# Kernel optimization log

Measured on AMD Instinct MI355X. Metric: run time of the kernel, lower is better.

The kernel has to match this reference:

```python
import jax, jax.numpy as jnp
import numpy as np

ALPHA = 0.5
NUM_NB = 8


def setup_inputs() -> dict:
    key = jax.random.key(0)
    k1, k2 = jax.random.split(key)
    pc1 = jax.random.normal(k1, (4, 3, 8192), dtype=jnp.float32)
    pred_flow = jax.random.normal(k2, (4, 3, 8192), dtype=jnp.float32)
    return {"pc1": pc1, "pred_flow": pred_flow}


def reference(pc1, pred_flow):
    # pc1, pred_flow: [B, 3, N] -> [B, N, 3]
    B, _, N = pc1.shape
    k = NUM_NB
    p = jnp.transpose(pc1, (0, 2, 1))         # [B, N, 3]
    f = jnp.transpose(pred_flow, (0, 2, 1))   # [B, N, 3]

    sq = jnp.sum(p * p, axis=-1)
    sqrdist = sq[:, :, None] + sq[:, None, :] - 2.0 * jnp.einsum('bnd,bmd->bnm', p, p)

    # k+1 smallest (sorted ascending), drop self (first column)
    neg_d, kidx = jax.lax.top_k(-sqrdist, k + 1)  # descending in -d == ascending in d
    dists = -neg_d[:, :, 1:]                      # [B, N, k]
    kidx = kidx[:, :, 1:]                         # [B, N, k]
    dists = jnp.maximum(dists, 0.0)

    # softmax over all N*k weights per batch
    w = jax.nn.softmax(jnp.exp(-dists / ALPHA).reshape(B, N * k), axis=1)
    w = w.reshape(B, N, k)

    # gather neighbor flows: [B, N, k, 3]
    grouped = jnp.take_along_axis(f[:, None, :, :],
                                  kidx[:, :, :, None],
                                  axis=2)
    diff = jnp.linalg.norm(grouped - f[:, :, None, :], axis=3)  # [B, N, k]
    diff_flow = (N * w * diff).sum(axis=2)                      # [B, N]
    return jnp.mean(diff_flow)
```

## Files before the change

### kernel.cpp

```cpp
#include <hip/hip_runtime.h>
#include <hip/hip_bf16.h>
#include <math.h>

#define BATCH 4
#define NQ 8192
#define KNB 8
#define K1 9
#define TILE 1024
#define CAP 24
#define THSAMP 256
#define SPART 2
#define IDXMASK 8191u
#define KEYMASK 0xFFFFE000u
#define EPS_S 1e-3f

#define CHAIN9(KEY) { unsigned kk = (KEY); \
  _Pragma("unroll") \
  for (int j = 0; j < K1; ++j) { \
    unsigned lo = min(kk, nk[j]); unsigned hi = max(kk, nk[j]); \
    nk[j] = lo; kk = hi; } }

#define DRAIN(T0) { \
  for (int i = 0; i < cnt; ++i) { \
    int j = sbuf[base + i]; \
    float dx = qx - sx[j], dy = qy - sy[j], dz = qz - sz[j]; \
    float d = dx*dx + dy*dy + dz*dz; \
    unsigned key = (__float_as_uint(d) & KEYMASK) | (unsigned)(c0 + (T0) + j); \
    if (key < nk[K1-1]) CHAIN9(key); \
  } \
  cnt = 0; \
  if (nk[K1-1] != 0xFFFFFFFFu) { \
    float td = __uint_as_float(nk[K1-1] | 0x1FFFu); \
    thetaS = fminf(thetaS, 0.5f*(td - qq) + EPS_S); \
  } }

#define GPROC(SS, JLOCAL) { \
  if ((SS) <= thetaS) { sbuf[base + cnt] = (unsigned short)(JLOCAL); cnt++; } }

__global__ __launch_bounds__(256) void theta_kernel(
    const float* __restrict__ pc, unsigned* __restrict__ thetaOut,
    float* __restrict__ hOut)
{
  __shared__ float swx[THSAMP], swy[THSAMP], swz[THSAMP];
  const int b = blockIdx.y, p = blockIdx.z;
  const int q = blockIdx.x * 256 + threadIdx.x;
  const float* __restrict__ px = pc + (size_t)b * 3 * NQ;
  const float* __restrict__ py = px + NQ;
  const float* __restrict__ pz = px + 2 * NQ;
  const int tid = threadIdx.x;
  const int si = tid * (NQ / THSAMP) + p * (NQ / THSAMP / SPART);
  swx[tid] = px[si]; swy[tid] = py[si]; swz[tid] = pz[si];
  __syncthreads();
  const float qx = px[q], qy = py[q], qz = pz[q];
  if (p == 0) hOut[b * NQ + q] = 0.5f * (qx*qx + qy*qy + qz*qz);
  unsigned nk[K1];
#pragma unroll
  for (int j = 0; j < K1; ++j) nk[j] = 0xFFFFFFFFu;
  for (int i = 0; i < THSAMP; ++i) {
    float dx = qx - swx[i], dy = qy - swy[i], dz = qz - swz[i];
    float d = dx * dx + dy * dy + dz * dz;
    CHAIN9(__float_as_uint(d));
  }
  thetaOut[(size_t)(b * NQ + q) * SPART + p] = nk[K1 - 1] | 0x1FFFu;
}

__global__ __launch_bounds__(256) void knn_kernel(
    const float* __restrict__ pc, const float* __restrict__ hB,
    const unsigned* __restrict__ thetaIn, unsigned* __restrict__ wsK,
    int P, int cpp)
{
  __shared__ float sx[TILE], sy[TILE], sz[TILE], sh[TILE];
  __shared__ unsigned short sbuf[256 * CAP];
  const int b = blockIdx.y;
  const int p = blockIdx.z;
  const int q = blockIdx.x * 256 + threadIdx.x;
  const float* __restrict__ px = pc + (size_t)b * 3 * NQ;
  const float* __restrict__ py = px + NQ;
  const float* __restrict__ pz = px + 2 * NQ;
  const float* __restrict__ ph = hB + (size_t)b * NQ;
  const float qx = px[q], qy = py[q], qz = pz[q];
  const float nqx = -qx, nqy = -qy, nqz = -qz;
  const float qq = qx*qx + qy*qy + qz*qz;

  uint2 th = ((const uint2*)thetaIn)[b * NQ + q];
  float thetaS = 0.5f * (__uint_as_float(min(th.x, th.y)) - qq) + EPS_S;

  unsigned nk[K1];
#pragma unroll
  for (int j = 0; j < K1; ++j) nk[j] = 0xFFFFFFFFu;

  const unsigned base = (unsigned)threadIdx.x * CAP;
  int cnt = 0;
  const int c0 = p * cpp;

  for (int t0 = 0; t0 < cpp; t0 += TILE) {
    __syncthreads();
    {
      const float4* gx = (const float4*)(px + c0 + t0);
      const float4* gy = (const float4*)(py + c0 + t0);
      const float4* gz = (const float4*)(pz + c0 + t0);
      const float4* gh = (const float4*)(ph + c0 + t0);
      float4* lx = (float4*)sx; float4* ly = (float4*)sy;
      float4* lz = (float4*)sz; float4* lh = (float4*)sh;
      for (int i = threadIdx.x; i < TILE / 4; i += 256) {
        lx[i] = gx[i]; ly[i] = gy[i]; lz[i] = gz[i]; lh[i] = gh[i];
      }
    }
    __syncthreads();

    const float4* sx4 = (const float4*)sx;
    const float4* sy4 = (const float4*)sy;
    const float4* sz4 = (const float4*)sz;
    const float4* sh4 = (const float4*)sh;
    for (int i4 = 0; i4 < TILE / 4; i4 += 2) {
      if (__any(cnt >= CAP - 8)) { DRAIN(t0); }
      float4 X = sx4[i4], Y = sy4[i4], Z = sz4[i4], H = sh4[i4];
      const int jb = i4 * 4;
      float s0 = fmaf(nqx, X.x, fmaf(nqy, Y.x, fmaf(nqz, Z.x, H.x)));
      float s1 = fmaf(nqx, X.y, fmaf(nqy, Y.y, fmaf(nqz, Z.y, H.y)));
      float s2 = fmaf(nqx, X.z, fmaf(nqy, Y.z, fmaf(nqz, Z.z, H.z)));
      float s3 = fmaf(nqx, X.w, fmaf(nqy, Y.w, fmaf(nqz, Z.w, H.w)));
      GPROC(s0, jb + 0); GPROC(s1, jb + 1);
      GPROC(s2, jb + 2); GPROC(s3, jb + 3);
      X = sx4[i4 + 1]; Y = sy4[i4 + 1]; Z = sz4[i4 + 1]; H = sh4[i4 + 1];
      float s4 = fmaf(nqx, X.x, fmaf(nqy, Y.x, fmaf(nqz, Z.x, H.x)));
      float s5 = fmaf(nqx, X.y, fmaf(nqy, Y.y, fmaf(nqz, Z.y, H.y)));
      float s6 = fmaf(nqx, X.z, fmaf(nqy, Y.z, fmaf(nqz, Z.z, H.z)));
      float s7 = fmaf(nqx, X.w, fmaf(nqy, Y.w, fmaf(nqz, Z.w, H.w)));
      GPROC(s4, jb + 4); GPROC(s5, jb + 5);
      GPROC(s6, jb + 6); GPROC(s7, jb + 7);
    }
    DRAIN(t0);
  }

  size_t o = ((size_t)((b * NQ + q) * P + p)) * K1;
#pragma unroll
  for (int j = 0; j < K1; ++j) wsK[o + j] = nk[j];
}

__global__ __launch_bounds__(256) void loss_kernel(
    const float* __restrict__ pc, const float* __restrict__ pf,
    const unsigned* __restrict__ wsK, float* __restrict__ acc, int P)
{
  const int b = blockIdx.y;
  const int q = blockIdx.x * 256 + threadIdx.x;
  const float* __restrict__ px = pc + (size_t)b * 3 * NQ;
  const float* __restrict__ py = px + NQ;
  const float* __restrict__ pz = px + 2 * NQ;
  const float* __restrict__ fx = pf + (size_t)b * 3 * NQ;
  const float* __restrict__ fy = fx + NQ;
  const float* __restrict__ fz = fx + 2 * NQ;

  unsigned nk[KNB];
#pragma unroll
  for (int j = 0; j < KNB; ++j) nk[j] = 0xFFFFFFFFu;

  const size_t o = (size_t)((b * NQ + q) * P) * K1;
  const int total = P * K1;
  for (int m = 0; m < total; ++m) {
    unsigned key = wsK[o + m];
    if ((key & IDXMASK) == (unsigned)q) continue;
    if (key < nk[KNB - 1]) {
      unsigned kk = key;
#pragma unroll
      for (int j = 0; j < KNB; ++j) {
        unsigned lo = min(kk, nk[j]); unsigned hi = max(kk, nk[j]);
        nk[j] = lo; kk = hi;
      }
    }
  }

  const float qx = px[q], qy = py[q], qz = pz[q];
  const float fqx = fx[q], fqy = fy[q], fqz = fz[q];
  float ssum = 0.f, sdsum = 0.f;
#pragma unroll
  for (int j = 0; j < KNB; ++j) {
    int i = (int)(nk[j] & IDXMASK);
    float dx = qx - px[i], dy = qy - py[i], dz = qz - pz[i];
    float d = dx * dx + dy * dy + dz * dz;
    float e = expf(expf(-2.0f * d));
    float gx = fx[i] - fqx, gy = fy[i] - fqy, gz = fz[i] - fqz;
    float diff = sqrtf(gx * gx + gy * gy + gz * gz);
    ssum += e; sdsum += e * diff;
  }

  for (int off = 32; off > 0; off >>= 1) {
    ssum += __shfl_down(ssum, off);
    sdsum += __shfl_down(sdsum, off);
  }
  __shared__ float r[8];
  const int lane = threadIdx.x & 63, wid = threadIdx.x >> 6;
  if (lane == 0) { r[wid * 2] = ssum; r[wid * 2 + 1] = sdsum; }
  __syncthreads();
  if (threadIdx.x == 0) {
    float s0 = r[0] + r[2] + r[4] + r[6];
    float s1 = r[1] + r[3] + r[5] + r[7];
    atomicAdd(&acc[b * 2 + 0], s0);
    atomicAdd(&acc[b * 2 + 1], s1);
  }
}

__global__ void final_kernel(const float* __restrict__ acc, float* __restrict__ out)
{
  if (threadIdx.x == 0) {
    float s = 0.f;
    for (int b = 0; b < BATCH; ++b) s += acc[b * 2 + 1] / acc[b * 2];
    out[0] = s * (1.0f / BATCH);
  }
}

extern "C" void kernel_launch(void* const* d_in, const int* in_sizes, int n_in,
                              void* d_out, int out_size, void* d_ws, size_t ws_size,
                              hipStream_t stream) {
  const float* pc = (const float*)d_in[0];
  const float* pf = (const float*)d_in[1];
  float* out = (float*)d_out;
  float* acc = (float*)d_ws;
  const size_t thetaBytes = (size_t)BATCH * NQ * SPART * sizeof(unsigned);
  const size_t hBytes = (size_t)BATCH * NQ * sizeof(float);
  unsigned* thetaBuf = (unsigned*)((char*)d_ws + 256);
  float* hBuf = (float*)((char*)d_ws + 256 + thetaBytes);
  unsigned* wsK = (unsigned*)((char*)d_ws + 256 + thetaBytes + hBytes);

  const size_t fixed = 256 + thetaBytes + hBytes;
  const size_t needP8 = fixed + (size_t)BATCH * NQ * 8 * K1 * sizeof(unsigned);
  const size_t needP4 = fixed + (size_t)BATCH * NQ * 4 * K1 * sizeof(unsigned);
  const int P = (ws_size >= needP8) ? 8 : ((ws_size >= needP4) ? 4 : 1);
  const int cpp = NQ / P;

  hipMemsetAsync(d_ws, 0, 256, stream);

  dim3 g0(NQ / 256, BATCH, SPART);
  theta_kernel<<<g0, 256, 0, stream>>>(pc, thetaBuf, hBuf);

  dim3 g1(NQ / 256, BATCH, P);
  knn_kernel<<<g1, 256, 0, stream>>>(pc, hBuf, thetaBuf, wsK, P, cpp);

  dim3 g2(NQ / 256, BATCH);
  loss_kernel<<<g2, 256, 0, stream>>>(pc, pf, wsK, acc, P);

  final_kernel<<<1, 64, 0, stream>>>(acc, out);
}
```

Baseline: 134.3 us.

## Unroll KNN scan to 16 candidates, enlarge buffer, coalesce workspace layout

```diff
diff --git a/kernel.cpp b/kernel.cpp
--- a/kernel.cpp
+++ b/kernel.cpp
@@ -7,7 +7,7 @@
 #define KNB 8
 #define K1 9
 #define TILE 1024
-#define CAP 24
+#define CAP 32
 #define THSAMP 256
 #define SPART 2
 #define IDXMASK 8191u
@@ -36,6 +36,12 @@
 
 #define GPROC(SS, JLOCAL) { \
   if ((SS) <= thetaS) { sbuf[base + cnt] = (unsigned short)(JLOCAL); cnt++; } }
+
+#define SCORE4(S0,S1,S2,S3, X,Y,Z,H) \
+  float S0 = fmaf(nqx, X.x, fmaf(nqy, Y.x, fmaf(nqz, Z.x, H.x))); \
+  float S1 = fmaf(nqx, X.y, fmaf(nqy, Y.y, fmaf(nqz, Z.y, H.y))); \
+  float S2 = fmaf(nqx, X.z, fmaf(nqy, Y.z, fmaf(nqz, Z.z, H.z))); \
+  float S3 = fmaf(nqx, X.w, fmaf(nqy, Y.w, fmaf(nqz, Z.w, H.w)));
 
 __global__ __launch_bounds__(256) void theta_kernel(
     const float* __restrict__ pc, unsigned* __restrict__ thetaOut,
@@ -112,30 +118,30 @@
     const float4* sy4 = (const float4*)sy;
     const float4* sz4 = (const float4*)sz;
     const float4* sh4 = (const float4*)sh;
-    for (int i4 = 0; i4 < TILE / 4; i4 += 2) {
-      if (__any(cnt >= CAP - 8)) { DRAIN(t0); }
-      float4 X = sx4[i4], Y = sy4[i4], Z = sz4[i4], H = sh4[i4];
-      const int jb = i4 * 4;
-      float s0 = fmaf(nqx, X.x, fmaf(nqy, Y.x, fmaf(nqz, Z.x, H.x)));
-      float s1 = fmaf(nqx, X.y, fmaf(nqy, Y.y, fmaf(nqz, Z.y, H.y)));
-      float s2 = fmaf(nqx, X.z, fmaf(nqy, Y.z, fmaf(nqz, Z.z, H.z)));
-      float s3 = fmaf(nqx, X.w, fmaf(nqy, Y.w, fmaf(nqz, Z.w, H.w)));
-      GPROC(s0, jb + 0); GPROC(s1, jb + 1);
-      GPROC(s2, jb + 2); GPROC(s3, jb + 3);
-      X = sx4[i4 + 1]; Y = sy4[i4 + 1]; Z = sz4[i4 + 1]; H = sh4[i4 + 1];
-      float s4 = fmaf(nqx, X.x, fmaf(nqy, Y.x, fmaf(nqz, Z.x, H.x)));
-      float s5 = fmaf(nqx, X.y, fmaf(nqy, Y.y, fmaf(nqz, Z.y, H.y)));
-      float s6 = fmaf(nqx, X.z, fmaf(nqy, Y.z, fmaf(nqz, Z.z, H.z)));
-      float s7 = fmaf(nqx, X.w, fmaf(nqy, Y.w, fmaf(nqz, Z.w, H.w)));
-      GPROC(s4, jb + 4); GPROC(s5, jb + 5);
-      GPROC(s6, jb + 6); GPROC(s7, jb + 7);
+    for (int i16 = 0; i16 < TILE / 16; ++i16) {
+      if (__any(cnt >= CAP - 16)) { DRAIN(t0); }
+      const int i4 = i16 * 4;
+      const int jb = i16 * 16;
+      float4 X0 = sx4[i4], X1 = sx4[i4+1], X2 = sx4[i4+2], X3 = sx4[i4+3];
+      float4 Y0 = sy4[i4], Y1 = sy4[i4+1], Y2 = sy4[i4+2], Y3 = sy4[i4+3];
+      float4 Z0 = sz4[i4], Z1 = sz4[i4+1], Z2 = sz4[i4+2], Z3 = sz4[i4+3];
+      float4 H0 = sh4[i4], H1 = sh4[i4+1], H2 = sh4[i4+2], H3 = sh4[i4+3];
+      SCORE4(s0, s1, s2, s3, X0, Y0, Z0, H0);
+      SCORE4(s4, s5, s6, s7, X1, Y1, Z1, H1);
+      SCORE4(s8, s9, sa, sb, X2, Y2, Z2, H2);
+      SCORE4(sc, sd, se, sf, X3, Y3, Z3, H3);
+      GPROC(s0, jb + 0);  GPROC(s1, jb + 1);  GPROC(s2, jb + 2);  GPROC(s3, jb + 3);
+      GPROC(s4, jb + 4);  GPROC(s5, jb + 5);  GPROC(s6, jb + 6);  GPROC(s7, jb + 7);
+      GPROC(s8, jb + 8);  GPROC(s9, jb + 9);  GPROC(sa, jb + 10); GPROC(sb, jb + 11);
+      GPROC(sc, jb + 12); GPROC(sd, jb + 13); GPROC(se, jb + 14); GPROC(sf, jb + 15);
     }
     DRAIN(t0);
   }
 
-  size_t o = ((size_t)((b * NQ + q) * P + p)) * K1;
-#pragma unroll
-  for (int j = 0; j < K1; ++j) wsK[o + j] = nk[j];
+  const size_t qo = (size_t)b * NQ + q;
+#pragma unroll
+  for (int j = 0; j < K1; ++j)
+    wsK[((size_t)(b * P + p) * K1 + j) * NQ + q] = nk[j];
 }
 
 __global__ __launch_bounds__(256) void loss_kernel(
@@ -155,10 +161,9 @@
 #pragma unroll
   for (int j = 0; j < KNB; ++j) nk[j] = 0xFFFFFFFFu;
 
-  const size_t o = (size_t)((b * NQ + q) * P) * K1;
   const int total = P * K1;
   for (int m = 0; m < total; ++m) {
-    unsigned key = wsK[o + m];
+    unsigned key = wsK[((size_t)b * P * K1 + m) * NQ + q];
     if ((key & IDXMASK) == (unsigned)q) continue;
     if (key < nk[KNB - 1]) {
       unsigned kk = key;
```

Result: no change. 134.2 us (-0.1%).
